# Performance work log

Measured on AMD Instinct MI355X. Metric: run time of the kernel, lower is better.

Reference implementation:

```python
import jax, jax.numpy as jnp
import numpy as np

INPUT_DIM = 512
SLOT_DIM = 256
MEM_SLOTS = 64

def setup_inputs() -> dict:
    key = jax.random.key(0)
    ks = jax.random.split(key, 6)
    B, S = 16, 4096
    sequence = jax.random.normal(ks[0], (B, S, INPUT_DIM), dtype=jnp.float32)
    # encoder Linear(input_dim -> slot_dim)
    enc_w = jax.random.normal(ks[1], (SLOT_DIM, INPUT_DIM), dtype=jnp.float32) / np.sqrt(INPUT_DIM)
    enc_b = jnp.zeros((SLOT_DIM,), dtype=jnp.float32)
    # memory bank
    mem = jax.random.normal(ks[2], (MEM_SLOTS, SLOT_DIM), dtype=jnp.float32) * 0.1
    # decoder Linear(slot_dim -> input_dim)
    dec_w = jax.random.normal(ks[3], (INPUT_DIM, SLOT_DIM), dtype=jnp.float32) / np.sqrt(SLOT_DIM)
    dec_b = jnp.zeros((INPUT_DIM,), dtype=jnp.float32)
    return {"sequence": sequence, "enc_w": enc_w, "enc_b": enc_b,
            "mem": mem, "dec_w": dec_w, "dec_b": dec_b}

def reference(sequence, enc_w, enc_b, mem, dec_w, dec_b):
    # encode: [B,S,D] @ [D,Dk] -> tanh
    encoded = jnp.tanh(jnp.einsum('bsd,kd->bsk', sequence, enc_w) + enc_b)
    scale = jnp.sqrt(jnp.asarray(encoded.shape[-1], encoded.dtype))
    # attention over memory slots: [B,S,M]
    attention = jax.nn.softmax(jnp.einsum('bsk,mk->bsm', encoded, mem) / scale, axis=-1)
    # weighted read: [B,S,Dk]
    memory = jnp.einsum('bsm,mk->bsk', attention, mem)
    # decode: [B,S,D]
    reconstruction = jnp.einsum('bsk,dk->bsd', memory, dec_w) + dec_b
    return reconstruction, attention, memory
```

## Files before the change

### kernel.cpp

```cpp
#include <hip/hip_runtime.h>
#include <hip/hip_bf16.h>

#define IN_DIM  512
#define SL_DIM  256
#define M_SLOTS 64
#define TILE_R  64

typedef __attribute__((ext_vector_type(8))) short  short8;
typedef __attribute__((ext_vector_type(4))) float  f32x4;

__device__ __forceinline__ short f2bf(float f) {
  union { float f; unsigned u; } v; v.f = f;
  unsigned r = (v.u + 0x7FFFu + ((v.u >> 16) & 1u)) >> 16;
  return (short)r;
}

__device__ __forceinline__ unsigned cvt2(float lo, float hi) {
  union { __hip_bfloat162 h; unsigned u; } c;
  c.h = __float22bfloat162_rn(make_float2(lo, hi));
  return c.u;
}

__device__ __forceinline__ short8 pack8(float4 v0, float4 v1) {
  union { unsigned u[4]; short8 s; } r;
  r.u[0] = cvt2(v0.x, v0.y);
  r.u[1] = cvt2(v0.z, v0.w);
  r.u[2] = cvt2(v1.x, v1.y);
  r.u[3] = cvt2(v1.z, v1.w);
  return r.s;
}

__device__ __forceinline__ float fast_tanh(float x) {
  x = fminf(15.f, fmaxf(-15.f, x));
  float e = __expf(2.f * x);
  return (e - 1.f) / (e + 1.f);
}

__global__ void convert_weights(const float* __restrict__ enc_w,
                                const float* __restrict__ dec_w,
                                const float* __restrict__ mem,
                                short* __restrict__ encb, short* __restrict__ decb,
                                short* __restrict__ memb, short* __restrict__ memTb) {
  int i = blockIdx.x * 256 + threadIdx.x;
  encb[i] = f2bf(enc_w[i]);
  decb[i] = f2bf(dec_w[i]);
  if (i < M_SLOTS * SL_DIM) {
    short v = f2bf(mem[i]);
    memb[i] = v;
    memTb[(i & 255) * M_SLOTS + (i >> 8)] = v;
  }
}

__global__ __launch_bounds__(256, 3) void fused_kernel(
    const float* __restrict__ seq, const float* __restrict__ enc_b,
    const float* __restrict__ dec_b, const short* __restrict__ encw,
    const short* __restrict__ decw, const short* __restrict__ memb,
    const short* __restrict__ memTb, float* __restrict__ out) {
  const int tid  = threadIdx.x;
  const int wave = tid >> 6;
  const int lane = tid & 63;
  const int l16  = lane & 15;
  const int quad = lane >> 4;
  const int r0   = blockIdx.x * TILE_R;

  __shared__ __align__(16) short Ebuf[TILE_R][SL_DIM + 8];
  __shared__ __align__(16) short Pbuf[TILE_R][M_SLOTS + 8];

  float* __restrict__ outR = out;
  float* __restrict__ outA = out + 33554432;
  float* __restrict__ outM = out + 37748736;

  f32x4 acc[4][4];
#pragma unroll
  for (int rb = 0; rb < 4; ++rb)
#pragma unroll
    for (int cb = 0; cb < 4; ++cb) acc[rb][cb] = (f32x4){0.f, 0.f, 0.f, 0.f};

  const float* aP[4];
  const short* bP[4];
#pragma unroll
  for (int rb = 0; rb < 4; ++rb)
    aP[rb] = seq + (size_t)(r0 + 16 * rb + l16) * IN_DIM + quad * 8;
#pragma unroll
  for (int cb = 0; cb < 4; ++cb)
    bP[cb] = encw + (64 * wave + 16 * cb + l16) * IN_DIM + quad * 8;

  for (int kt = 0; kt < 16; ++kt) {
    const int k0 = kt * 32;
    short8 a[4], b[4];
#pragma unroll
    for (int rb = 0; rb < 4; ++rb) {
      float4 v0 = *(const float4*)(aP[rb] + k0);
      float4 v1 = *(const float4*)(aP[rb] + k0 + 4);
      a[rb] = pack8(v0, v1);
    }
#pragma unroll
    for (int cb = 0; cb < 4; ++cb)
      b[cb] = *(const short8*)(bP[cb] + k0);
#pragma unroll
    for (int rb = 0; rb < 4; ++rb)
#pragma unroll
      for (int cb = 0; cb < 4; ++cb)
        acc[rb][cb] = __builtin_amdgcn_mfma_f32_16x16x32_bf16(a[rb], b[cb], acc[rb][cb], 0, 0, 0);
  }

#pragma unroll
  for (int cb = 0; cb < 4; ++cb) {
    int col = 64 * wave + 16 * cb + l16;
    float bias = enc_b[col];
#pragma unroll
    for (int rb = 0; rb < 4; ++rb)
#pragma unroll
      for (int r = 0; r < 4; ++r) {
        int row = 16 * rb + quad * 4 + r;
        Ebuf[row][col] = f2bf(fast_tanh(acc[rb][cb][r] + bias));
      }
  }
  __syncthreads();

  f32x4 acc2[4];
#pragma unroll
  for (int nb = 0; nb < 4; ++nb) acc2[nb] = (f32x4){0.f, 0.f, 0.f, 0.f};
  const int g2row = 16 * wave + l16;
#pragma unroll
  for (int kt = 0; kt < 8; ++kt) {
    int k0 = kt * 32;
    short8 a = *(const short8*)&Ebuf[g2row][k0 + quad * 8];
#pragma unroll
    for (int nb = 0; nb < 4; ++nb) {
      short8 b = *(const short8*)(memb + (16 * nb + l16) * SL_DIM + k0 + quad * 8);
      acc2[nb] = __builtin_amdgcn_mfma_f32_16x16x32_bf16(a, b, acc2[nb], 0, 0, 0);
    }
  }
#pragma unroll
  for (int r = 0; r < 4; ++r) {
    int lrow = 16 * wave + quad * 4 + r;
    float s0 = acc2[0][r] * 0.0625f, s1 = acc2[1][r] * 0.0625f;
    float s2 = acc2[2][r] * 0.0625f, s3 = acc2[3][r] * 0.0625f;
    float mx = fmaxf(fmaxf(s0, s1), fmaxf(s2, s3));
    for (int off = 1; off < 16; off <<= 1) mx = fmaxf(mx, __shfl_xor(mx, off));
    float e0 = __expf(s0 - mx), e1 = __expf(s1 - mx);
    float e2 = __expf(s2 - mx), e3 = __expf(s3 - mx);
    float sum = e0 + e1 + e2 + e3;
    for (int off = 1; off < 16; off <<= 1) sum += __shfl_xor(sum, off);
    float inv = 1.0f / sum;
    float p0 = e0 * inv, p1 = e1 * inv, p2 = e2 * inv, p3 = e3 * inv;
    size_t grow = (size_t)(r0 + lrow) * M_SLOTS;
    outA[grow + 0  + l16] = p0;  Pbuf[lrow][0  + l16] = f2bf(p0);
    outA[grow + 16 + l16] = p1;  Pbuf[lrow][16 + l16] = f2bf(p1);
    outA[grow + 32 + l16] = p2;  Pbuf[lrow][32 + l16] = f2bf(p2);
    outA[grow + 48 + l16] = p3;  Pbuf[lrow][48 + l16] = f2bf(p3);
  }
  __syncthreads();

  f32x4 acc3[4][4];
#pragma unroll
  for (int rb = 0; rb < 4; ++rb)
#pragma unroll
    for (int cb = 0; cb < 4; ++cb) acc3[rb][cb] = (f32x4){0.f, 0.f, 0.f, 0.f};
#pragma unroll
  for (int kt = 0; kt < 2; ++kt) {
    int k0 = kt * 32;
    short8 a[4], b[4];
#pragma unroll
    for (int rb = 0; rb < 4; ++rb)
      a[rb] = *(const short8*)&Pbuf[16 * rb + l16][k0 + quad * 8];
#pragma unroll
    for (int cb = 0; cb < 4; ++cb) {
      int n = 64 * wave + 16 * cb + l16;
      b[cb] = *(const short8*)(memTb + n * M_SLOTS + k0 + quad * 8);
    }
#pragma unroll
    for (int rb = 0; rb < 4; ++rb)
#pragma unroll
      for (int cb = 0; cb < 4; ++cb)
        acc3[rb][cb] = __builtin_amdgcn_mfma_f32_16x16x32_bf16(a[rb], b[cb], acc3[rb][cb], 0, 0, 0);
  }
#pragma unroll
  for (int cb = 0; cb < 4; ++cb) {
    int col = 64 * wave + 16 * cb + l16;
#pragma unroll
    for (int rb = 0; rb < 4; ++rb)
#pragma unroll
      for (int r = 0; r < 4; ++r) {
        int row = 16 * rb + quad * 4 + r;
        float v = acc3[rb][cb][r];
        outM[(size_t)(r0 + row) * SL_DIM + col] = v;
        Ebuf[row][col] = f2bf(v);
      }
  }
  __syncthreads();

  for (int h = 0; h < 2; ++h) {
    const int c0 = 128 * wave + 64 * h;
    f32x4 acc4[4][4];
#pragma unroll
    for (int rb = 0; rb < 4; ++rb)
#pragma unroll
      for (int cb = 0; cb < 4; ++cb) acc4[rb][cb] = (f32x4){0.f, 0.f, 0.f, 0.f};
#pragma unroll
    for (int kt = 0; kt < 8; ++kt) {
      int k0 = kt * 32;
      short8 a[4], b[4];
#pragma unroll
      for (int rb = 0; rb < 4; ++rb)
        a[rb] = *(const short8*)&Ebuf[16 * rb + l16][k0 + quad * 8];
#pragma unroll
      for (int cb = 0; cb < 4; ++cb) {
        int n = c0 + 16 * cb + l16;
        b[cb] = *(const short8*)(decw + n * SL_DIM + k0 + quad * 8);
      }
#pragma unroll
      for (int rb = 0; rb < 4; ++rb)
#pragma unroll
        for (int cb = 0; cb < 4; ++cb)
          acc4[rb][cb] = __builtin_amdgcn_mfma_f32_16x16x32_bf16(a[rb], b[cb], acc4[rb][cb], 0, 0, 0);
    }
#pragma unroll
    for (int cb = 0; cb < 4; ++cb) {
      int col = c0 + 16 * cb + l16;
      float bias = dec_b[col];
#pragma unroll
      for (int rb = 0; rb < 4; ++rb)
#pragma unroll
        for (int r = 0; r < 4; ++r) {
          int row = 16 * rb + quad * 4 + r;
          outR[(size_t)(r0 + row) * IN_DIM + col] = acc4[rb][cb][r] + bias;
        }
    }
  }
}

extern "C" void kernel_launch(void* const* d_in, const int* in_sizes, int n_in,
                              void* d_out, int out_size, void* d_ws, size_t ws_size,
                              hipStream_t stream) {
  const float* seq   = (const float*)d_in[0];
  const float* enc_w = (const float*)d_in[1];
  const float* enc_b = (const float*)d_in[2];
  const float* mem   = (const float*)d_in[3];
  const float* dec_w = (const float*)d_in[4];
  const float* dec_b = (const float*)d_in[5];
  float* out = (float*)d_out;

  char* ws = (char*)d_ws;
  short* encb  = (short*)(ws);
  short* decb  = (short*)(ws + 262144);
  short* memb  = (short*)(ws + 524288);
  short* memTb = (short*)(ws + 557056);

  convert_weights<<<512, 256, 0, stream>>>(enc_w, dec_w, mem, encb, decb, memb, memTb);
  fused_kernel<<<1024, 256, 0, stream>>>(seq, enc_b, dec_b, encb, decb, memb, memTb, out);
}
```

Before: 420.9 us.

## Halve row tile, stage sequence through double-buffered LDS, raise occupancy

Cuts the row tile from 64 to 32 rows and doubles the grid, with launch bounds raised to 6 blocks per CU so fewer registers are needed and occupancy goes up. The sequence tile is now loaded cooperatively with coalesced float4 loads, converted to bf16, and written into a double-buffered LDS tile that is prefetched one k-step ahead. Previously each wave loaded the A fragments redundantly from global memory. The cost is a barrier in every k-iteration, and only two waves do the attention/softmax stage. Each block also re-reads the encoder and decoder weights for fewer rows, which doubles weight traffic.

```diff
diff --git a/kernel.cpp b/kernel.cpp
--- a/kernel.cpp
+++ b/kernel.cpp
@@ -4,7 +4,7 @@
 #define IN_DIM  512
 #define SL_DIM  256
 #define M_SLOTS 64
-#define TILE_R  64
+#define TILE_R  32
 
 typedef __attribute__((ext_vector_type(8))) short  short8;
 typedef __attribute__((ext_vector_type(4))) float  f32x4;
@@ -19,15 +19,6 @@
   union { __hip_bfloat162 h; unsigned u; } c;
   c.h = __float22bfloat162_rn(make_float2(lo, hi));
   return c.u;
-}
-
-__device__ __forceinline__ short8 pack8(float4 v0, float4 v1) {
-  union { unsigned u[4]; short8 s; } r;
-  r.u[0] = cvt2(v0.x, v0.y);
-  r.u[1] = cvt2(v0.z, v0.w);
-  r.u[2] = cvt2(v1.x, v1.y);
-  r.u[3] = cvt2(v1.z, v1.w);
-  return r.s;
 }
 
 __device__ __forceinline__ float fast_tanh(float x) {
@@ -51,7 +42,7 @@
   }
 }
 
-__global__ __launch_bounds__(256, 3) void fused_kernel(
+__global__ __launch_bounds__(256, 6) void fused_kernel(
     const float* __restrict__ seq, const float* __restrict__ enc_b,
     const float* __restrict__ dec_b, const short* __restrict__ encw,
     const short* __restrict__ decw, const short* __restrict__ memb,
@@ -63,6 +54,7 @@
   const int quad = lane >> 4;
   const int r0   = blockIdx.x * TILE_R;
 
+  __shared__ __align__(16) short As[2][TILE_R][44];
   __shared__ __align__(16) short Ebuf[TILE_R][SL_DIM + 8];
   __shared__ __align__(16) short Pbuf[TILE_R][M_SLOTS + 8];
 
@@ -70,35 +62,46 @@
   float* __restrict__ outA = out + 33554432;
   float* __restrict__ outM = out + 37748736;
 
-  f32x4 acc[4][4];
-#pragma unroll
-  for (int rb = 0; rb < 4; ++rb)
+  f32x4 acc[2][4];
+#pragma unroll
+  for (int rb = 0; rb < 2; ++rb)
 #pragma unroll
     for (int cb = 0; cb < 4; ++cb) acc[rb][cb] = (f32x4){0.f, 0.f, 0.f, 0.f};
 
-  const float* aP[4];
+  const int srow = tid >> 3;
+  const int skc  = (tid & 7) * 4;
+  const float* sp = seq + (size_t)(r0 + srow) * IN_DIM + skc;
   const short* bP[4];
-#pragma unroll
-  for (int rb = 0; rb < 4; ++rb)
-    aP[rb] = seq + (size_t)(r0 + 16 * rb + l16) * IN_DIM + quad * 8;
 #pragma unroll
   for (int cb = 0; cb < 4; ++cb)
     bP[cb] = encw + (64 * wave + 16 * cb + l16) * IN_DIM + quad * 8;
 
+  {
+    float4 v = *(const float4*)(sp);
+    uint2 w; w.x = cvt2(v.x, v.y); w.y = cvt2(v.z, v.w);
+    *(uint2*)&As[0][srow][skc] = w;
+  }
+
   for (int kt = 0; kt < 16; ++kt) {
-    const int k0 = kt * 32;
-    short8 a[4], b[4];
-#pragma unroll
-    for (int rb = 0; rb < 4; ++rb) {
-      float4 v0 = *(const float4*)(aP[rb] + k0);
-      float4 v1 = *(const float4*)(aP[rb] + k0 + 4);
-      a[rb] = pack8(v0, v1);
-    }
+    const int k0  = kt * 32;
+    const int cur = kt & 1;
+    float4 vn;
+    if (kt < 15) vn = *(const float4*)(sp + k0 + 32);
+    short8 b[4];
 #pragma unroll
     for (int cb = 0; cb < 4; ++cb)
       b[cb] = *(const short8*)(bP[cb] + k0);
-#pragma unroll
-    for (int rb = 0; rb < 4; ++rb)
+    __syncthreads();
+    if (kt < 15) {
+      uint2 w; w.x = cvt2(vn.x, vn.y); w.y = cvt2(vn.z, vn.w);
+      *(uint2*)&As[cur ^ 1][srow][skc] = w;
+    }
+    short8 a[2];
+#pragma unroll
+    for (int rb = 0; rb < 2; ++rb)
+      a[rb] = *(const short8*)&As[cur][16 * rb + l16][quad * 8];
+#pragma unroll
+    for (int rb = 0; rb < 2; ++rb)
 #pragma unroll
       for (int cb = 0; cb < 4; ++cb)
         acc[rb][cb] = __builtin_amdgcn_mfma_f32_16x16x32_bf16(a[rb], b[cb], acc[rb][cb], 0, 0, 0);
@@ -109,7 +112,7 @@
     int col = 64 * wave + 16 * cb + l16;
     float bias = enc_b[col];
 #pragma unroll
-    for (int rb = 0; rb < 4; ++rb)
+    for (int rb = 0; rb < 2; ++rb)
 #pragma unroll
       for (int r = 0; r < 4; ++r) {
         int row = 16 * rb + quad * 4 + r;
@@ -118,52 +121,54 @@
   }
   __syncthreads();
 
-  f32x4 acc2[4];
-#pragma unroll
-  for (int nb = 0; nb < 4; ++nb) acc2[nb] = (f32x4){0.f, 0.f, 0.f, 0.f};
-  const int g2row = 16 * wave + l16;
-#pragma unroll
-  for (int kt = 0; kt < 8; ++kt) {
-    int k0 = kt * 32;
-    short8 a = *(const short8*)&Ebuf[g2row][k0 + quad * 8];
-#pragma unroll
-    for (int nb = 0; nb < 4; ++nb) {
-      short8 b = *(const short8*)(memb + (16 * nb + l16) * SL_DIM + k0 + quad * 8);
-      acc2[nb] = __builtin_amdgcn_mfma_f32_16x16x32_bf16(a, b, acc2[nb], 0, 0, 0);
-    }
-  }
-#pragma unroll
-  for (int r = 0; r < 4; ++r) {
-    int lrow = 16 * wave + quad * 4 + r;
-    float s0 = acc2[0][r] * 0.0625f, s1 = acc2[1][r] * 0.0625f;
-    float s2 = acc2[2][r] * 0.0625f, s3 = acc2[3][r] * 0.0625f;
-    float mx = fmaxf(fmaxf(s0, s1), fmaxf(s2, s3));
-    for (int off = 1; off < 16; off <<= 1) mx = fmaxf(mx, __shfl_xor(mx, off));
-    float e0 = __expf(s0 - mx), e1 = __expf(s1 - mx);
-    float e2 = __expf(s2 - mx), e3 = __expf(s3 - mx);
-    float sum = e0 + e1 + e2 + e3;
-    for (int off = 1; off < 16; off <<= 1) sum += __shfl_xor(sum, off);
-    float inv = 1.0f / sum;
-    float p0 = e0 * inv, p1 = e1 * inv, p2 = e2 * inv, p3 = e3 * inv;
-    size_t grow = (size_t)(r0 + lrow) * M_SLOTS;
-    outA[grow + 0  + l16] = p0;  Pbuf[lrow][0  + l16] = f2bf(p0);
-    outA[grow + 16 + l16] = p1;  Pbuf[lrow][16 + l16] = f2bf(p1);
-    outA[grow + 32 + l16] = p2;  Pbuf[lrow][32 + l16] = f2bf(p2);
-    outA[grow + 48 + l16] = p3;  Pbuf[lrow][48 + l16] = f2bf(p3);
+  if (wave < 2) {
+    f32x4 acc2[4];
+#pragma unroll
+    for (int nb = 0; nb < 4; ++nb) acc2[nb] = (f32x4){0.f, 0.f, 0.f, 0.f};
+    const int g2row = 16 * wave + l16;
+#pragma unroll
+    for (int kt = 0; kt < 8; ++kt) {
+      int k0 = kt * 32;
+      short8 a = *(const short8*)&Ebuf[g2row][k0 + quad * 8];
+#pragma unroll
+      for (int nb = 0; nb < 4; ++nb) {
+        short8 b = *(const short8*)(memb + (16 * nb + l16) * SL_DIM + k0 + quad * 8);
+        acc2[nb] = __builtin_amdgcn_mfma_f32_16x16x32_bf16(a, b, acc2[nb], 0, 0, 0);
+      }
+    }
+#pragma unroll
+    for (int r = 0; r < 4; ++r) {
+      int lrow = 16 * wave + quad * 4 + r;
+      float s0 = acc2[0][r] * 0.0625f, s1 = acc2[1][r] * 0.0625f;
+      float s2 = acc2[2][r] * 0.0625f, s3 = acc2[3][r] * 0.0625f;
+      float mx = fmaxf(fmaxf(s0, s1), fmaxf(s2, s3));
+      for (int off = 1; off < 16; off <<= 1) mx = fmaxf(mx, __shfl_xor(mx, off));
+      float e0 = __expf(s0 - mx), e1 = __expf(s1 - mx);
+      float e2 = __expf(s2 - mx), e3 = __expf(s3 - mx);
+      float sum = e0 + e1 + e2 + e3;
+      for (int off = 1; off < 16; off <<= 1) sum += __shfl_xor(sum, off);
+      float inv = 1.0f / sum;
+      float p0 = e0 * inv, p1 = e1 * inv, p2 = e2 * inv, p3 = e3 * inv;
+      size_t grow = (size_t)(r0 + lrow) * M_SLOTS;
+      outA[grow + 0  + l16] = p0;  Pbuf[lrow][0  + l16] = f2bf(p0);
+      outA[grow + 16 + l16] = p1;  Pbuf[lrow][16 + l16] = f2bf(p1);
+      outA[grow + 32 + l16] = p2;  Pbuf[lrow][32 + l16] = f2bf(p2);
+      outA[grow + 48 + l16] = p3;  Pbuf[lrow][48 + l16] = f2bf(p3);
+    }
   }
   __syncthreads();
 
-  f32x4 acc3[4][4];
-#pragma unroll
-  for (int rb = 0; rb < 4; ++rb)
+  f32x4 acc3[2][4];
+#pragma unroll
+  for (int rb = 0; rb < 2; ++rb)
 #pragma unroll
     for (int cb = 0; cb < 4; ++cb) acc3[rb][cb] = (f32x4){0.f, 0.f, 0.f, 0.f};
 #pragma unroll
   for (int kt = 0; kt < 2; ++kt) {
     int k0 = kt * 32;
-    short8 a[4], b[4];
-#pragma unroll
-    for (int rb = 0; rb < 4; ++rb)
+    short8 a[2], b[4];
+#pragma unroll
+    for (int rb = 0; rb < 2; ++rb)
       a[rb] = *(const short8*)&Pbuf[16 * rb + l16][k0 + quad * 8];
 #pragma unroll
     for (int cb = 0; cb < 4; ++cb) {
@@ -171,7 +176,7 @@
       b[cb] = *(const short8*)(memTb + n * M_SLOTS + k0 + quad * 8);
     }
 #pragma unroll
-    for (int rb = 0; rb < 4; ++rb)
+    for (int rb = 0; rb < 2; ++rb)
 #pragma unroll
       for (int cb = 0; cb < 4; ++cb)
         acc3[rb][cb] = __builtin_amdgcn_mfma_f32_16x16x32_bf16(a[rb], b[cb], acc3[rb][cb], 0, 0, 0);
@@ -180,7 +185,7 @@
   for (int cb = 0; cb < 4; ++cb) {
     int col = 64 * wave + 16 * cb + l16;
 #pragma unroll
-    for (int rb = 0; rb < 4; ++rb)
+    for (int rb = 0; rb < 2; ++rb)
 #pragma unroll
       for (int r = 0; r < 4; ++r) {
         int row = 16 * rb + quad * 4 + r;
@@ -193,17 +198,17 @@
 
   for (int h = 0; h < 2; ++h) {
     const int c0 = 128 * wave + 64 * h;
-    f32x4 acc4[4][4];
-#pragma unroll
-    for (int rb = 0; rb < 4; ++rb)
+    f32x4 acc4[2][4];
+#pragma unroll
+    for (int rb = 0; rb < 2; ++rb)
 #pragma unroll
       for (int cb = 0; cb < 4; ++cb) acc4[rb][cb] = (f32x4){0.f, 0.f, 0.f, 0.f};
 #pragma unroll
     for (int kt = 0; kt < 8; ++kt) {
       int k0 = kt * 32;
-      short8 a[4], b[4];
-#pragma unroll
-      for (int rb = 0; rb < 4; ++rb)
+      short8 a[2], b[4];
+#pragma unroll
+      for (int rb = 0; rb < 2; ++rb)
         a[rb] = *(const short8*)&Ebuf[16 * rb + l16][k0 + quad * 8];
 #pragma unroll
       for (int cb = 0; cb < 4; ++cb) {
@@ -211,7 +216,7 @@
         b[cb] = *(const short8*)(decw + n * SL_DIM + k0 + quad * 8);
       }
 #pragma unroll
-      for (int rb = 0; rb < 4; ++rb)
+      for (int rb = 0; rb < 2; ++rb)
 #pragma unroll
         for (int cb = 0; cb < 4; ++cb)
           acc4[rb][cb] = __builtin_amdgcn_mfma_f32_16x16x32_bf16(a[rb], b[cb], acc4[rb][cb], 0, 0, 0);
@@ -221,7 +226,7 @@
       int col = c0 + 16 * cb + l16;
       float bias = dec_b[col];
 #pragma unroll
-      for (int rb = 0; rb < 4; ++rb)
+      for (int rb = 0; rb < 2; ++rb)
 #pragma unroll
         for (int r = 0; r < 4; ++r) {
           int row = 16 * rb + quad * 4 + r;
@@ -249,5 +254,5 @@
   short* memTb = (short*)(ws + 557056);
 
   convert_weights<<<512, 256, 0, stream>>>(enc_w, dec_w, mem, encb, decb, memb, memTb);
-  fused_kernel<<<1024, 256, 0, stream>>>(seq, enc_b, dec_b, encb, decb, memb, memTb, out);
-}
+  fused_kernel<<<2048, 256, 0, stream>>>(seq, enc_b, dec_b, encb, decb, memb, memTb, out);
+}
```

Result: slower. 466.3 us (+10.8%).

## Stage sequence tile through double-buffered LDS with register prefetch in encoder GEMM

Applied to the files above, without the earlier changes.

The encoder GEMM no longer has all four waves each load and convert the whole 64-row sequence tile from global memory. Instead the block loads each 64-column K chunk once cooperatively, converts it to bf16, and stores it in a double-buffered LDS array that shares space with Pbuf. The next chunk is prefetched into registers while MFMAs run on the current one. This cuts redundant global loads and conversions by 4x and overlaps loads with compute, at the cost of a barrier per K step and extra LDS use that may lower occupancy.

```diff
diff --git a/kernel.cpp b/kernel.cpp
--- a/kernel.cpp
+++ b/kernel.cpp
@@ -19,15 +19,6 @@
   union { __hip_bfloat162 h; unsigned u; } c;
   c.h = __float22bfloat162_rn(make_float2(lo, hi));
   return c.u;
-}
-
-__device__ __forceinline__ short8 pack8(float4 v0, float4 v1) {
-  union { unsigned u[4]; short8 s; } r;
-  r.u[0] = cvt2(v0.x, v0.y);
-  r.u[1] = cvt2(v0.z, v0.w);
-  r.u[2] = cvt2(v1.x, v1.y);
-  r.u[3] = cvt2(v1.z, v1.w);
-  return r.s;
 }
 
 __device__ __forceinline__ float fast_tanh(float x) {
@@ -64,7 +55,10 @@
   const int r0   = blockIdx.x * TILE_R;
 
   __shared__ __align__(16) short Ebuf[TILE_R][SL_DIM + 8];
-  __shared__ __align__(16) short Pbuf[TILE_R][M_SLOTS + 8];
+  __shared__ __align__(16) union {
+    short As[2][TILE_R][72];
+    short Pbuf[TILE_R][M_SLOTS + 8];
+  } U;
 
   float* __restrict__ outR = out;
   float* __restrict__ outA = out + 33554432;
@@ -76,32 +70,61 @@
 #pragma unroll
     for (int cb = 0; cb < 4; ++cb) acc[rb][cb] = (f32x4){0.f, 0.f, 0.f, 0.f};
 
-  const float* aP[4];
+  const int srow = tid >> 2;
+  const int skc  = (tid & 3) * 16;
+  const float* sp = seq + (size_t)(r0 + srow) * IN_DIM + skc;
   const short* bP[4];
-#pragma unroll
-  for (int rb = 0; rb < 4; ++rb)
-    aP[rb] = seq + (size_t)(r0 + 16 * rb + l16) * IN_DIM + quad * 8;
 #pragma unroll
   for (int cb = 0; cb < 4; ++cb)
     bP[cb] = encw + (64 * wave + 16 * cb + l16) * IN_DIM + quad * 8;
 
-  for (int kt = 0; kt < 16; ++kt) {
-    const int k0 = kt * 32;
-    short8 a[4], b[4];
-#pragma unroll
-    for (int rb = 0; rb < 4; ++rb) {
-      float4 v0 = *(const float4*)(aP[rb] + k0);
-      float4 v1 = *(const float4*)(aP[rb] + k0 + 4);
-      a[rb] = pack8(v0, v1);
-    }
-#pragma unroll
-    for (int cb = 0; cb < 4; ++cb)
-      b[cb] = *(const short8*)(bP[cb] + k0);
-#pragma unroll
-    for (int rb = 0; rb < 4; ++rb)
+  float4 v[4];
+#pragma unroll
+  for (int j = 0; j < 4; ++j) v[j] = *(const float4*)(sp + 4 * j);
+  {
+    uint4 w0, w1;
+    w0.x = cvt2(v[0].x, v[0].y); w0.y = cvt2(v[0].z, v[0].w);
+    w0.z = cvt2(v[1].x, v[1].y); w0.w = cvt2(v[1].z, v[1].w);
+    w1.x = cvt2(v[2].x, v[2].y); w1.y = cvt2(v[2].z, v[2].w);
+    w1.z = cvt2(v[3].x, v[3].y); w1.w = cvt2(v[3].z, v[3].w);
+    *(uint4*)&U.As[0][srow][skc]     = w0;
+    *(uint4*)&U.As[0][srow][skc + 8] = w1;
+  }
+#pragma unroll
+  for (int j = 0; j < 4; ++j) v[j] = *(const float4*)(sp + 64 + 4 * j);
+
+  for (int kt = 0; kt < 8; ++kt) {
+    const int cur = kt & 1;
+    __syncthreads();
+    if (kt < 7) {
+      uint4 w0, w1;
+      w0.x = cvt2(v[0].x, v[0].y); w0.y = cvt2(v[0].z, v[0].w);
+      w0.z = cvt2(v[1].x, v[1].y); w0.w = cvt2(v[1].z, v[1].w);
+      w1.x = cvt2(v[2].x, v[2].y); w1.y = cvt2(v[2].z, v[2].w);
+      w1.z = cvt2(v[3].x, v[3].y); w1.w = cvt2(v[3].z, v[3].w);
+      *(uint4*)&U.As[cur ^ 1][srow][skc]     = w0;
+      *(uint4*)&U.As[cur ^ 1][srow][skc + 8] = w1;
+    }
+    if (kt < 6) {
+#pragma unroll
+      for (int j = 0; j < 4; ++j) v[j] = *(const float4*)(sp + (kt + 2) * 64 + 4 * j);
+    }
+#pragma unroll
+    for (int ks = 0; ks < 2; ++ks) {
+      const int k0 = kt * 64 + ks * 32;
+      short8 a[4], b[4];
 #pragma unroll
       for (int cb = 0; cb < 4; ++cb)
-        acc[rb][cb] = __builtin_amdgcn_mfma_f32_16x16x32_bf16(a[rb], b[cb], acc[rb][cb], 0, 0, 0);
+        b[cb] = *(const short8*)(bP[cb] + k0);
+#pragma unroll
+      for (int rb = 0; rb < 4; ++rb)
+        a[rb] = *(const short8*)&U.As[cur][16 * rb + l16][ks * 32 + quad * 8];
+#pragma unroll
+      for (int rb = 0; rb < 4; ++rb)
+#pragma unroll
+        for (int cb = 0; cb < 4; ++cb)
+          acc[rb][cb] = __builtin_amdgcn_mfma_f32_16x16x32_bf16(a[rb], b[cb], acc[rb][cb], 0, 0, 0);
+    }
   }
 
 #pragma unroll
@@ -146,10 +169,10 @@
     float inv = 1.0f / sum;
     float p0 = e0 * inv, p1 = e1 * inv, p2 = e2 * inv, p3 = e3 * inv;
     size_t grow = (size_t)(r0 + lrow) * M_SLOTS;
-    outA[grow + 0  + l16] = p0;  Pbuf[lrow][0  + l16] = f2bf(p0);
-    outA[grow + 16 + l16] = p1;  Pbuf[lrow][16 + l16] = f2bf(p1);
-    outA[grow + 32 + l16] = p2;  Pbuf[lrow][32 + l16] = f2bf(p2);
-    outA[grow + 48 + l16] = p3;  Pbuf[lrow][48 + l16] = f2bf(p3);
+    outA[grow + 0  + l16] = p0;  U.Pbuf[lrow][0  + l16] = f2bf(p0);
+    outA[grow + 16 + l16] = p1;  U.Pbuf[lrow][16 + l16] = f2bf(p1);
+    outA[grow + 32 + l16] = p2;  U.Pbuf[lrow][32 + l16] = f2bf(p2);
+    outA[grow + 48 + l16] = p3;  U.Pbuf[lrow][48 + l16] = f2bf(p3);
   }
   __syncthreads();
 
@@ -164,7 +187,7 @@
     short8 a[4], b[4];
 #pragma unroll
     for (int rb = 0; rb < 4; ++rb)
-      a[rb] = *(const short8*)&Pbuf[16 * rb + l16][k0 + quad * 8];
+      a[rb] = *(const short8*)&U.Pbuf[16 * rb + l16][k0 + quad * 8];
 #pragma unroll
     for (int cb = 0; cb < 4; ++cb) {
       int n = 64 * wave + 16 * cb + l16;
@@ -184,9 +207,9 @@
 #pragma unroll
       for (int r = 0; r < 4; ++r) {
         int row = 16 * rb + quad * 4 + r;
-        float v = acc3[rb][cb][r];
-        outM[(size_t)(r0 + row) * SL_DIM + col] = v;
-        Ebuf[row][col] = f2bf(v);
+        float v2 = acc3[rb][cb][r];
+        outM[(size_t)(r0 + row) * SL_DIM + col] = v2;
+        Ebuf[row][col] = f2bf(v2);
       }
   }
   __syncthreads();
```

Result: faster. 389.5 us (-7.5%).
